# Performance work log

Measured on AMD Instinct MI355X. Metric: run time of the kernel, lower is better.

Reference implementation:

```python
import jax, jax.numpy as jnp
import numpy as np

B, L, C = 8, 65536, 64   # Cin must equal filters (broadcast constraint in original code)
F = 64                   # filters
K_ = 3                   # kernel_size
DL = 256                 # latent dim
EPS = 1e-8


def setup_inputs() -> dict:
    key = jax.random.key(0)
    k1, k2, k3, k4 = jax.random.split(key, 4)
    data = jax.random.normal(k1, (B, L, C), dtype=jnp.float32)
    ltnt = jax.random.normal(k2, (B, DL), dtype=jnp.float32)
    # glorot_normal-style scaling for learned params
    kernel = jax.random.normal(k3, (K_, C, F), dtype=jnp.float32) * np.sqrt(2.0 / (C * K_ + F))
    Wd = jax.random.normal(k4, (DL, F), dtype=jnp.float32) * np.sqrt(2.0 / (DL + F))
    bd = jnp.zeros((F,), dtype=jnp.float32)
    return {"data": data, "ltnt": ltnt, "kernel": kernel, "Wd": Wd, "bd": bd}


def reference(data, ltnt, kernel, Wd, bd):
    # per-sample modulation scale from latent: s in [B, F] (F == Cin)
    s = jax.nn.softplus(ltnt @ Wd + bd) + 1.0
    # demodulation: d[b,f] = rsqrt(sum_{k,c} (kernel[k,c,f]*s[b,c])^2 + eps)
    d = jax.lax.rsqrt(jnp.einsum('kcf,bc->bf', kernel * kernel, s * s) + EPS)
    # fused equivalent of per-sample weight modulation:
    #   conv(x, kernel * s[b,c] * d[b,f]) == d[b,f] * conv(x * s[b,c], kernel)
    xm = data * s[:, None, :]                          # [B, L, C]
    y = jax.lax.conv_general_dilated(
        xm, kernel, window_strides=(1,), padding='SAME',
        dimension_numbers=('NWC', 'WIO', 'NWC'))       # [B, L, F]
    return y * d[:, None, :]
```

## Files before the change

kernel.cpp:

```cpp
#include <hip/hip_runtime.h>

#define BATCH 8
#define SEQ   65536
#define CH    64
#define FILT  64
#define DLAT  256

#define BLK_PER_B   128
#define ROWS_PER_BLK 512
#define TILE_ROWS    64
#define TILES        (ROWS_PER_BLK / TILE_ROWS)
#define AROWS        66
#define ACHUNKS      (AROWS * 8)

#define BAR() do { asm volatile("s_waitcnt lgkmcnt(0)" ::: "memory"); \
                   __builtin_amdgcn_s_barrier(); } while (0)

typedef __bf16 bfrag  __attribute__((ext_vector_type(8)));
typedef float  floatx4 __attribute__((ext_vector_type(4)));

__global__ __launch_bounds__(256) void prep_kernel(
    const float* __restrict__ ltnt, const float* __restrict__ ker,
    const float* __restrict__ Wd,   const float* __restrict__ bd,
    __bf16* __restrict__ kmod)
{
    int b = blockIdx.x, tid = threadIdx.x;
    __shared__ float red[4][64];
    __shared__ float s_sh[64];
    __shared__ float d_sh[64];
    int f = tid & 63, p = tid >> 6;

    float sum = 0.f;
    #pragma unroll 8
    for (int j = p * 64; j < p * 64 + 64; ++j)
        sum += ltnt[b * DLAT + j] * Wd[j * FILT + f];
    red[p][f] = sum;
    __syncthreads();
    if (tid < 64) {
        float tot = red[0][tid] + red[1][tid] + red[2][tid] + red[3][tid] + bd[tid];
        float sp = (tot > 20.f) ? tot : log1pf(expf(tot));
        s_sh[tid] = sp + 1.f;
    }
    __syncthreads();

    float s2 = 0.f;
    for (int k = 0; k < 3; ++k)
        #pragma unroll
        for (int c = p * 16; c < p * 16 + 16; ++c) {
            float w = ker[k * 4096 + c * 64 + f];
            float sc = s_sh[c];
            s2 += w * w * sc * sc;
        }
    __syncthreads();
    red[p][f] = s2;
    __syncthreads();
    if (tid < 64) {
        float tot = red[0][tid] + red[1][tid] + red[2][tid] + red[3][tid];
        d_sh[tid] = rsqrtf(tot + 1e-8f);
    }
    __syncthreads();

    for (int o = tid; o < 3 * 64 * 64; o += 256) {
        int k = o >> 12, ff = (o >> 6) & 63, c = o & 63;
        kmod[b * 12288 + o] = (__bf16)(ker[k * 4096 + c * 64 + ff] * s_sh[c] * d_sh[ff]);
    }
}

__device__ __forceinline__ float4 scale4(float4 v, float s) {
    v.x *= s; v.y *= s; v.z *= s; v.w *= s; return v;
}

__device__ __forceinline__ bfrag cvt8(float4 a, float4 b) {
    bfrag r;
    r[0] = (__bf16)a.x; r[1] = (__bf16)a.y; r[2] = (__bf16)a.z; r[3] = (__bf16)a.w;
    r[4] = (__bf16)b.x; r[5] = (__bf16)b.y; r[6] = (__bf16)b.z; r[7] = (__bf16)b.w;
    return r;
}

__device__ __forceinline__ void stage_load(float4 pre[3][2],
                                           const float* __restrict__ xb,
                                           int r0, int tid) {
    #pragma unroll
    for (int i = 0; i < 3; ++i) {
        int id  = i * 256 + tid;
        int rho = id >> 3, c = id & 7;
        int g   = r0 - 1 + rho;
        bool ok = (id < ACHUNKS) && ((unsigned)g < (unsigned)SEQ);
        const float* p = xb + (size_t)(ok ? g : 0) * CH + c * 8;
        float s = ok ? 1.f : 0.f;
        pre[i][0] = scale4(*(const float4*)p, s);
        pre[i][1] = scale4(*(const float4*)(p + 4), s);
    }
}

__device__ __forceinline__ void stage_write(__bf16* __restrict__ A,
                                            float4 pre[3][2], int tid) {
    #pragma unroll
    for (int i = 0; i < 3; ++i) {
        int id = i * 256 + tid;
        if (id < ACHUNKS) {
            int rho = id >> 3, c = id & 7;
            int idx = (rho * 64 + c * 8) ^ ((rho & 7) << 3);
            *(bfrag*)(A + idx) = cvt8(pre[i][0], pre[i][1]);
        }
    }
}

__global__ __launch_bounds__(256, 4) void conv_kernel(
    const float* __restrict__ data, const __bf16* __restrict__ kmod,
    float* __restrict__ out)
{
    __shared__ __bf16 Abuf[2][AROWS * 64];
    __shared__ float  OutT[64 * 64];

    int tid  = threadIdx.x;
    int b    = blockIdx.x >> 7;
    int blk  = blockIdx.x & (BLK_PER_B - 1);
    int wave = tid >> 6, lane = tid & 63;
    int m = lane & 15, q = lane >> 4;

    const __bf16* kb = kmod + b * 12288;
    bfrag Bf[3][2];
    #pragma unroll
    for (int k = 0; k < 3; ++k)
        #pragma unroll
        for (int h = 0; h < 2; ++h)
            Bf[k][h] = *(const bfrag*)(kb + (k * 64 + wave * 16 + m) * 64 + h * 32 + q * 8);

    const float* xb = data + (size_t)b * SEQ * CH;
    float*       ob = out  + (size_t)b * SEQ * FILT;
    int base = blk * ROWS_PER_BLK;

    float4 pre[3][2];
    stage_load(pre, xb, base, tid);

    #pragma unroll 1
    for (int t = 0; t < TILES; ++t) {
        int r0 = base + t * TILE_ROWS;
        __bf16* A = Abuf[t & 1];

        stage_write(A, pre, tid);
        BAR();

        if (t + 1 < TILES)
            stage_load(pre, xb, r0 + TILE_ROWS, tid);

        floatx4 acc[4];
        #pragma unroll
        for (int rt = 0; rt < 4; ++rt) acc[rt] = floatx4{0, 0, 0, 0};

        #pragma unroll
        for (int rt = 0; rt < 4; ++rt) {
            #pragma unroll
            for (int k = 0; k < 3; ++k)
                #pragma unroll
                for (int h = 0; h < 2; ++h) {
                    int rho = rt * 16 + m + k;
                    bfrag a = *(const bfrag*)(A +
                        ((rho * 64 + h * 32 + q * 8) ^ ((rho & 7) << 3)));
                    acc[rt] = __builtin_amdgcn_mfma_f32_16x16x32_bf16(
                        a, Bf[k][h], acc[rt], 0, 0, 0);
                }
        }

        #pragma unroll
        for (int rt = 0; rt < 4; ++rt)
            #pragma unroll
            for (int r = 0; r < 4; ++r) {
                int row = rt * 16 + q * 4 + r;
                int col = (wave * 16 + m) ^ (q << 4);
                OutT[row * 64 + col] = acc[rt][r];
            }
        BAR();

        #pragma unroll
        for (int it = 0; it < 4; ++it) {
            int id  = it * 256 + tid;
            int row = id >> 4, c = id & 15;
            int scol = (c * 4) ^ (((row >> 2) & 3) << 4);
            floatx4 v = *(const floatx4*)(OutT + row * 64 + scol);
            *(floatx4*)(ob + (size_t)(r0 + row) * FILT + c * 4) = v;
        }
    }
}

extern "C" void kernel_launch(void* const* d_in, const int* in_sizes, int n_in,
                              void* d_out, int out_size, void* d_ws, size_t ws_size,
                              hipStream_t stream) {
    const float* data = (const float*)d_in[0];
    const float* ltnt = (const float*)d_in[1];
    const float* ker  = (const float*)d_in[2];
    const float* Wd   = (const float*)d_in[3];
    const float* bd   = (const float*)d_in[4];
    float* out = (float*)d_out;

    __bf16* kmod = (__bf16*)d_ws;

    prep_kernel<<<BATCH, 256, 0, stream>>>(ltnt, ker, Wd, bd, kmod);
    conv_kernel<<<BATCH * BLK_PER_B, 256, 0, stream>>>(data, kmod, out);
}
```

Measured before the change: 263.6 us.

## Swap MFMA operands for direct 2x2 tiled output stores without LDS transpose

Each wave now computes a 32-row by 32-filter block as a 2x2 set of MFMA tiles instead of 64 rows by 16 filters. The A and B operands are swapped so the accumulator holds four consecutive filters per lane, which lets each lane store a float4 straight to global memory. This removes the OutT shared-memory staging buffer and one barrier per tile, and each A fragment read from LDS is reused across two MFMAs. In exchange, global stores become 16-byte writes spread across rows rather than fully coalesced row writes, and each wave holds twice as many B fragments in registers.

```diff
diff --git a/kernel.cpp b/kernel.cpp
--- a/kernel.cpp
+++ b/kernel.cpp
@@ -111,21 +111,24 @@
     float* __restrict__ out)
 {
     __shared__ __bf16 Abuf[2][AROWS * 64];
-    __shared__ float  OutT[64 * 64];
 
     int tid  = threadIdx.x;
     int b    = blockIdx.x >> 7;
     int blk  = blockIdx.x & (BLK_PER_B - 1);
     int wave = tid >> 6, lane = tid & 63;
     int m = lane & 15, q = lane >> 4;
+    int wr = wave >> 1, wf = wave & 1;
 
     const __bf16* kb = kmod + b * 12288;
-    bfrag Bf[3][2];
+    bfrag Bf[2][3][2];
     #pragma unroll
-    for (int k = 0; k < 3; ++k)
+    for (int nt = 0; nt < 2; ++nt)
         #pragma unroll
-        for (int h = 0; h < 2; ++h)
-            Bf[k][h] = *(const bfrag*)(kb + (k * 64 + wave * 16 + m) * 64 + h * 32 + q * 8);
+        for (int k = 0; k < 3; ++k)
+            #pragma unroll
+            for (int h = 0; h < 2; ++h)
+                Bf[nt][k][h] = *(const bfrag*)(kb +
+                    (k * 64 + wf * 32 + nt * 16 + m) * 64 + h * 32 + q * 8);
 
     const float* xb = data + (size_t)b * SEQ * CH;
     float*       ob = out  + (size_t)b * SEQ * FILT;
@@ -145,41 +148,36 @@
         if (t + 1 < TILES)
             stage_load(pre, xb, r0 + TILE_ROWS, tid);
 
-        floatx4 acc[4];
+        floatx4 acc[2][2];
         #pragma unroll
-        for (int rt = 0; rt < 4; ++rt) acc[rt] = floatx4{0, 0, 0, 0};
+        for (int rt = 0; rt < 2; ++rt)
+            #pragma unroll
+            for (int nt = 0; nt < 2; ++nt)
+                acc[rt][nt] = floatx4{0, 0, 0, 0};
 
         #pragma unroll
-        for (int rt = 0; rt < 4; ++rt) {
+        for (int rt = 0; rt < 2; ++rt) {
             #pragma unroll
             for (int k = 0; k < 3; ++k)
                 #pragma unroll
                 for (int h = 0; h < 2; ++h) {
-                    int rho = rt * 16 + m + k;
+                    int rho = wr * 32 + rt * 16 + m + k;
                     bfrag a = *(const bfrag*)(A +
                         ((rho * 64 + h * 32 + q * 8) ^ ((rho & 7) << 3)));
-                    acc[rt] = __builtin_amdgcn_mfma_f32_16x16x32_bf16(
-                        a, Bf[k][h], acc[rt], 0, 0, 0);
+                    #pragma unroll
+                    for (int nt = 0; nt < 2; ++nt)
+                        acc[rt][nt] = __builtin_amdgcn_mfma_f32_16x16x32_bf16(
+                            Bf[nt][k][h], a, acc[rt][nt], 0, 0, 0);
                 }
         }
 
         #pragma unroll
-        for (int rt = 0; rt < 4; ++rt)
+        for (int rt = 0; rt < 2; ++rt) {
+            int row = r0 + wr * 32 + rt * 16 + m;
             #pragma unroll
-            for (int r = 0; r < 4; ++r) {
-                int row = rt * 16 + q * 4 + r;
-                int col = (wave * 16 + m) ^ (q << 4);
-                OutT[row * 64 + col] = acc[rt][r];
-            }
-        BAR();
-
-        #pragma unroll
-        for (int it = 0; it < 4; ++it) {
-            int id  = it * 256 + tid;
-            int row = id >> 4, c = id & 15;
-            int scol = (c * 4) ^ (((row >> 2) & 3) << 4);
-            floatx4 v = *(const floatx4*)(OutT + row * 64 + scol);
-            *(floatx4*)(ob + (size_t)(r0 + row) * FILT + c * 4) = v;
+            for (int nt = 0; nt < 2; ++nt)
+                *(floatx4*)(ob + (size_t)row * FILT + wf * 32 + nt * 16 + q * 4)
+                    = acc[rt][nt];
         }
     }
 }
```

After: 262.2 us. No clear change (-0.5%).
